# Performance work log

Measured on AMD Instinct MI355X. Metric: run time of the kernel, lower is better.

The kernel has to match this reference:

```python
import jax, jax.numpy as jnp
import numpy as np

D_IN = 1024
D_OUT = 1024
NUM_HEADS = 16
HEAD_DIM = D_OUT // NUM_HEADS


def setup_inputs() -> dict:
    key = jax.random.key(0)
    ks = jax.random.split(key, 6)
    s = 0.02
    return {
        "x": jax.random.normal(ks[0], (4, 2048, D_IN), dtype=jnp.float32),
        "W_q": jax.random.normal(ks[1], (D_IN, D_OUT), dtype=jnp.float32) * s,
        "W_k": jax.random.normal(ks[2], (D_IN, D_OUT), dtype=jnp.float32) * s,
        "W_v": jax.random.normal(ks[3], (D_IN, D_OUT), dtype=jnp.float32) * s,
        "W_o": jax.random.normal(ks[4], (D_OUT, D_OUT), dtype=jnp.float32) * s,
        "b_o": jax.random.normal(ks[5], (D_OUT,), dtype=jnp.float32) * s,
    }


def reference(x, W_q, W_k, W_v, W_o, b_o):
    b, n, _ = x.shape
    # project and split heads: [b, h, n, d]
    q = (x @ W_q).reshape(b, n, NUM_HEADS, HEAD_DIM).transpose(0, 2, 1, 3)
    k = (x @ W_k).reshape(b, n, NUM_HEADS, HEAD_DIM).transpose(0, 2, 1, 3)
    v = (x @ W_v).reshape(b, n, NUM_HEADS, HEAD_DIM).transpose(0, 2, 1, 3)
    scores = jnp.einsum("bhqd,bhkd->bhqk", q, k)
    causal = jnp.tril(jnp.ones((n, n), dtype=bool))  # True = keep
    scores = jnp.where(causal, scores, -jnp.inf)
    attn = jax.nn.softmax(scores / np.sqrt(HEAD_DIM).astype(np.float32), axis=-1)
    ctx = jnp.einsum("bhqk,bhkd->bhqd", attn, v)
    ctx = ctx.transpose(0, 2, 1, 3).reshape(b, n, D_OUT)
    return ctx @ W_o + b_o
```

## Files before the change

kernel.cpp:

```cpp
#include <hip/hip_runtime.h>
#include <hip/hip_bf16.h>

#define NHEADS 16
#define HDIM 64
#define SEQ 2048
#define BATCH 4
#define DMODEL 1024
#define MTOT (BATCH * SEQ)

typedef short v8s __attribute__((ext_vector_type(8)));
typedef short v4s __attribute__((ext_vector_type(4)));
typedef float v4f __attribute__((ext_vector_type(4)));
typedef float v16f __attribute__((ext_vector_type(16)));
typedef unsigned int v4u __attribute__((ext_vector_type(4)));
typedef unsigned short u16;
typedef unsigned int u32;

__device__ __forceinline__ u16 f2bf(float f) {
    union { float f; unsigned u; } v; v.f = f;
    unsigned r = v.u + 0x7FFFu + ((v.u >> 16) & 1u);
    return (u16)(r >> 16);
}

__device__ __forceinline__ void g2l16(const u16* g, short* l) {
    __builtin_amdgcn_global_load_lds(
        (const __attribute__((address_space(1))) u32*)g,
        (__attribute__((address_space(3))) u32*)l, 16, 0, 0);
}

__device__ __forceinline__ unsigned pk_bf16(float a, float b) {
    unsigned r;
    asm("v_cvt_pk_bf16_f32 %0, %1, %2" : "=v"(r) : "v"(a), "v"(b));
    return r;
}
__device__ __forceinline__ void pl32swap(unsigned& x, unsigned& y) {
    asm("v_permlane32_swap_b32 %0, %1" : "+v"(x), "+v"(y));
}
__device__ __forceinline__ v8s build_pa(float a0, float a1, float a2, float a3,
                                        float b0, float b1, float b2, float b3) {
    unsigned X  = pk_bf16(a0, a1);
    unsigned X2 = pk_bf16(a2, a3);
    unsigned Y  = pk_bf16(b0, b1);
    unsigned Y2 = pk_bf16(b2, b3);
    pl32swap(X, Y);
    pl32swap(X2, Y2);
    v4u w; w[0] = X; w[1] = X2; w[2] = Y; w[3] = Y2;
    return __builtin_bit_cast(v8s, w);
}

__device__ __forceinline__ void transpose_body(
    const float* __restrict__ src, u16* __restrict__ dst, int k0, int n0)
{
    __shared__ __align__(8) short Ts[64 * 68];
    const int t = threadIdx.x;
    const int n4 = (t & 15) * 4, kl = t >> 4;
#pragma unroll
    for (int it = 0; it < 4; ++it) {
        int k = kl + 16 * it;
        v4f v = *(const v4f*)&src[(size_t)(k0 + k) * DMODEL + n0 + n4];
        v4s p;
#pragma unroll
        for (int e = 0; e < 4; ++e) p[e] = (short)f2bf(v[e]);
        *(v4s*)&Ts[k * 68 + n4] = p;
    }
    __syncthreads();
    const int nl = t >> 4, k4 = (t & 15) * 4;
#pragma unroll
    for (int it = 0; it < 4; ++it) {
        int n = nl + 16 * it;
        v4s o;
#pragma unroll
        for (int e = 0; e < 4; ++e) o[e] = Ts[(k4 + e) * 68 + n];
        *(v4s*)&dst[(size_t)(n0 + n) * DMODEL + k0 + k4] = o;
    }
}

__global__ __launch_bounds__(256)
void transpose_w(const float* __restrict__ src, u16* __restrict__ dst)
{
    transpose_body(src, dst, blockIdx.x * 64, blockIdx.y * 64);
}

__global__ __launch_bounds__(256)
void prep(const float* __restrict__ x, u16* __restrict__ xb,
          const float* __restrict__ s0, const float* __restrict__ s1,
          const float* __restrict__ s2, const float* __restrict__ s3,
          u16* __restrict__ wdst)
{
    const int blk = blockIdx.x;
    if (blk < 1024) {
        const int z = blk >> 8;
        const int rem = blk & 255;
        const float* src = (z == 0) ? s0 : (z == 1) ? s1 : (z == 2) ? s2 : s3;
        transpose_body(src, wdst + (size_t)z * DMODEL * DMODEL,
                       (rem & 15) * 64, (rem >> 4) * 64);
    } else {
        size_t i = ((size_t)(blk - 1024) * 256 + threadIdx.x) * 8;
        v4f a = *(const v4f*)&x[i];
        v4f b = *(const v4f*)&x[i + 4];
        v8s p;
#pragma unroll
        for (int e = 0; e < 4; ++e) p[e] = (short)f2bf(a[e]);
#pragma unroll
        for (int e = 0; e < 4; ++e) p[4 + e] = (short)f2bf(b[e]);
        *(v8s*)&xb[i] = p;
    }
}

#define QSCALE (0.125f * 1.44269504088896f)

__device__ __forceinline__ void qkv_epilogue(
    v4f (&acc)[4][4], int which, int n0, int m0, int wn, int wm,
    int l15, int quad, u16* Qb, u16* Kb, u16* Vt)
{
    if (which == 2) {
#pragma unroll
        for (int i = 0; i < 4; ++i)
#pragma unroll
            for (int j = 0; j < 4; ++j) {
                int col = n0 + wn + j * 16 + l15;
                int h = col >> 6, d = col & 63;
                int m = m0 + wm + i * 16 + quad * 4;
                int b = m >> 11, n = m & (SEQ - 1);
                v4s pv;
#pragma unroll
                for (int r = 0; r < 4; ++r) pv[r] = (short)f2bf(acc[i][j][r]);
                *(v4s*)&Vt[((size_t)(b * NHEADS + h) * HDIM + d) * SEQ + n] = pv;
            }
    } else {
        u16* Ob = (which == 0) ? Qb : Kb;
        const float scale = (which == 0) ? QSCALE : 1.0f;
#pragma unroll
        for (int i = 0; i < 4; ++i)
#pragma unroll
            for (int j = 0; j < 4; ++j) {
                int col = n0 + wn + j * 16 + l15;
                int h = col >> 6, d = col & 63;
#pragma unroll
                for (int r = 0; r < 4; ++r) {
                    int m = m0 + wm + i * 16 + quad * 4 + r;
                    int b = m >> 11, n = m & (SEQ - 1);
                    Ob[((size_t)(b * NHEADS + h) * SEQ + n) * HDIM + d] =
                        f2bf(acc[i][j][r] * scale);
                }
            }
    }
}

__global__ __launch_bounds__(256, 2)
void qkv_fast(const u16* __restrict__ xb, const u16* __restrict__ Wt,
              u16* __restrict__ Qb, u16* __restrict__ Kb, u16* __restrict__ Vt)
{
    __shared__ __align__(16) short As[128 * 128];
    __shared__ __align__(16) short Bs[128 * 128];

    const int which = blockIdx.z;
    const u16* W = Wt + (size_t)which * DMODEL * DMODEL;

    const int n0 = blockIdx.x * 128;
    const int m0 = blockIdx.y * 128;
    const int t = threadIdx.x;
    const int lane = t & 63;
    const int l15 = lane & 15;
    const int quad = lane >> 4;
    const int wave = t >> 6;
    const int wm = (wave >> 1) * 64;
    const int wn = (wave & 1) * 64;
    const int srow = t >> 4;
    const int sc8 = (t & 15) * 8;

    v4f acc[4][4];
#pragma unroll
    for (int i = 0; i < 4; ++i)
#pragma unroll
        for (int j = 0; j < 4; ++j) acc[i][j] = {0.f, 0.f, 0.f, 0.f};

    for (int k0 = 0; k0 < DMODEL; k0 += 128) {
        __syncthreads();
#pragma unroll
        for (int c = 0; c < 8; ++c) {
            g2l16(&xb[(size_t)(m0 + c * 16 + srow) * DMODEL + k0 + sc8],
                  &As[(c * 16 + srow) * 128 + sc8]);
            g2l16(&W[(size_t)(n0 + c * 16 + srow) * DMODEL + k0 + sc8],
                  &Bs[(c * 16 + srow) * 128 + sc8]);
        }
        __syncthreads();

#pragma unroll
        for (int kh = 0; kh < 4; ++kh) {
            v8s af[4], bf[4];
#pragma unroll
            for (int i = 0; i < 4; ++i)
                af[i] = *(const v8s*)
                    &As[(wm + i * 16 + l15) * 128 + kh * 32 + quad * 8];
#pragma unroll
            for (int j = 0; j < 4; ++j)
                bf[j] = *(const v8s*)
                    &Bs[(wn + j * 16 + l15) * 128 + kh * 32 + quad * 8];
#pragma unroll
            for (int i = 0; i < 4; ++i)
#pragma unroll
                for (int j = 0; j < 4; ++j)
                    acc[i][j] = __builtin_amdgcn_mfma_f32_16x16x32_bf16(
                        af[i], bf[j], acc[i][j], 0, 0, 0);
        }
    }
    qkv_epilogue(acc, which, n0, m0, wn, wm, l15, quad, Qb, Kb, Vt);
}

__global__ __launch_bounds__(256, 2)
void qkv_slow(const float* __restrict__ x, const u16* __restrict__ Wt,
              u16* __restrict__ Qb, u16* __restrict__ Kb, u16* __restrict__ Vt)
{
    __shared__ __align__(16) short As[128 * 32];
    __shared__ __align__(16) short Bs[128 * 32];

    const int which = blockIdx.z;
    const u16* W = Wt + (size_t)which * DMODEL * DMODEL;

    const int n0 = blockIdx.x * 128;
    const int m0 = blockIdx.y * 128;
    const int t = threadIdx.x;
    const int lane = t & 63;
    const int l15 = lane & 15;
    const int quad = lane >> 4;
    const int wave = t >> 6;
    const int wm = (wave >> 1) * 64;
    const int wn = (wave & 1) * 64;
    const int srow = t >> 2;
    const int sc8 = (t & 3) * 8;

    v4f acc[4][4];
#pragma unroll
    for (int i = 0; i < 4; ++i)
#pragma unroll
        for (int j = 0; j < 4; ++j) acc[i][j] = {0.f, 0.f, 0.f, 0.f};

    for (int k0 = 0; k0 < DMODEL; k0 += 32) {
        __syncthreads();
        g2l16(&W[(size_t)(n0 + srow) * DMODEL + k0 + sc8], &Bs[srow * 32 + sc8]);
        g2l16(&W[(size_t)(n0 + 64 + srow) * DMODEL + k0 + sc8],
              &Bs[(64 + srow) * 32 + sc8]);
#pragma unroll
        for (int it = 0; it < 2; ++it) {
            int row = srow + 64 * it;
            const float* xp = &x[(size_t)(m0 + row) * DMODEL + k0 + sc8];
            v4f x0 = *(const v4f*)xp;
            v4f x1 = *(const v4f*)(xp + 4);
            v8s av;
#pragma unroll
            for (int e = 0; e < 4; ++e) av[e] = (short)f2bf(x0[e]);
#pragma unroll
            for (int e = 0; e < 4; ++e) av[4 + e] = (short)f2bf(x1[e]);
            *(v8s*)&As[row * 32 + sc8] = av;
        }
        __syncthreads();

        v8s af[4], bf[4];
#pragma unroll
        for (int i = 0; i < 4; ++i)
            af[i] = *(const v8s*)&As[(wm + i * 16 + l15) * 32 + quad * 8];
#pragma unroll
        for (int j = 0; j < 4; ++j)
            bf[j] = *(const v8s*)&Bs[(wn + j * 16 + l15) * 32 + quad * 8];
#pragma unroll
        for (int i = 0; i < 4; ++i)
#pragma unroll
            for (int j = 0; j < 4; ++j)
                acc[i][j] = __builtin_amdgcn_mfma_f32_16x16x32_bf16(
                    af[i], bf[j], acc[i][j], 0, 0, 0);
    }
    qkv_epilogue(acc, which, n0, m0, wn, wm, l15, quad, Qb, Kb, Vt);
}

#define VXOR(d) ((((d) & 7) << 1) | (((d) >> 3) & 1))

__global__ __launch_bounds__(256, 2)
void attn(const u16* __restrict__ Qb, const u16* __restrict__ Kb,
          const u16* __restrict__ Vt, u16* __restrict__ Cx)
{
    __shared__ __align__(16) short Ks[128 * 64];
    __shared__ __align__(16) short Vs[64 * 128];

    const int ell = blockIdx.x;
    const int xcd = ell & 7;
    const int rest = ell >> 3;
    const int p = rest & 7;
    const int bh = ((rest >> 3) << 3) | xcd;

    const int t = threadIdx.x;
    const int lane = t & 63;
    const int l31 = lane & 31;
    const int hi = lane >> 5;
    const int wave = t >> 6;
    const int koff = hi * 8;

    const u16* Qh = Qb + (size_t)bh * SEQ * HDIM;
    const u16* Kh = Kb + (size_t)bh * SEQ * HDIM;
    const u16* Vh = Vt + (size_t)bh * HDIM * SEQ;

    const int krow = t >> 3;
    const int kslot = t & 7;
    const int vrow = t >> 4;
    const int vslot = t & 15;
    const int b = bh >> 4, h = bh & 15;

#pragma unroll 1
    for (int phase = 0; phase < 2; ++phase) {
        const int qt = phase ? p : (15 - p);
        const int q0w = qt * 128 + wave * 32;

        v8s qf[4];
#pragma unroll
        for (int dc = 0; dc < 4; ++dc)
            qf[dc] = *(const v8s*)
                &Qh[(size_t)(q0w + l31) * HDIM + dc * 16 + koff];

        v16f o0, o1;
#pragma unroll
        for (int r = 0; r < 16; ++r) { o0[r] = 0.f; o1[r] = 0.f; }
        float ls = 0.f;

        v8s pk[4], pv[4];
#pragma unroll
        for (int it = 0; it < 4; ++it)
            pk[it] = *(const v8s*)
                &Kh[(size_t)(it * 32 + krow) * HDIM + kslot * 8];
#pragma unroll
        for (int it = 0; it < 4; ++it)
            pv[it] = *(const v8s*)
                &Vh[(size_t)(it * 16 + vrow) * SEQ + vslot * 8];

#pragma unroll 1
        for (int kb = 0; kb <= qt; ++kb) {
            __syncthreads();
#pragma unroll
            for (int it = 0; it < 4; ++it) {
                int row = it * 32 + krow;
                *(v8s*)&Ks[row * 64 + ((kslot ^ (row & 7)) << 3)] = pk[it];
            }
#pragma unroll
            for (int it = 0; it < 4; ++it) {
                int d = it * 16 + vrow;
                *(v8s*)&Vs[d * 128 + ((vslot ^ VXOR(d)) << 3)] = pv[it];
            }
            __syncthreads();

            if (kb < qt) {
                const int kn = (kb + 1) * 128;
#pragma unroll
                for (int it = 0; it < 4; ++it)
                    pk[it] = *(const v8s*)
                        &Kh[(size_t)(kn + it * 32 + krow) * HDIM + kslot * 8];
#pragma unroll
                for (int it = 0; it < 4; ++it)
                    pv[it] = *(const v8s*)
                        &Vh[(size_t)(it * 16 + vrow) * SEQ + kn + vslot * 8];
            }

#pragma unroll
            for (int k2 = 0; k2 < 2; ++k2) {
                const int kbase = kb * 128 + k2 * 64;
                if (kbase > q0w + 31) continue;
                const bool diag = (kbase + 63 > q0w);
                const int qrow = q0w + l31;

                v16f st0, st1;
#pragma unroll
                for (int r = 0; r < 16; ++r) { st0[r] = 0.f; st1[r] = 0.f; }
#pragma unroll
                for (int dc = 0; dc < 4; ++dc) {
                    const int ds = dc * 2 + hi;
                    const int r0 = k2 * 64 + l31;
                    const int r1 = k2 * 64 + 32 + l31;
                    v8s kf0 = *(const v8s*)
                        &Ks[r0 * 64 + ((ds ^ (r0 & 7)) << 3)];
                    v8s kf1 = *(const v8s*)
                        &Ks[r1 * 64 + ((ds ^ (r1 & 7)) << 3)];
                    st0 = __builtin_amdgcn_mfma_f32_32x32x16_bf16(
                        kf0, qf[dc], st0, 0, 0, 0);
                    st1 = __builtin_amdgcn_mfma_f32_32x32x16_bf16(
                        kf1, qf[dc], st1, 0, 0, 0);
                }

                v16f pe0, pe1;
                if (!diag) {
#pragma unroll
                    for (int r = 0; r < 16; ++r) {
                        pe0[r] = exp2f(st0[r]);
                        pe1[r] = exp2f(st1[r]);
                    }
                } else {
#pragma unroll
                    for (int r = 0; r < 16; ++r) {
                        int kl = kbase + (r & 3) + 8 * (r >> 2) + 4 * hi;
                        pe0[r] = (kl > qrow) ? 0.f : exp2f(st0[r]);
                        pe1[r] = (kl + 32 > qrow) ? 0.f : exp2f(st1[r]);
                    }
                }
#pragma unroll
                for (int r = 0; r < 16; ++r) ls += pe0[r] + pe1[r];

                v8s pa0 = build_pa(pe0[0], pe0[1], pe0[2], pe0[3],
                                   pe0[4], pe0[5], pe0[6], pe0[7]);
                v8s pa1 = build_pa(pe0[8], pe0[9], pe0[10], pe0[11],
                                   pe0[12], pe0[13], pe0[14], pe0[15]);
                v8s pa2 = build_pa(pe1[0], pe1[1], pe1[2], pe1[3],
                                   pe1[4], pe1[5], pe1[6], pe1[7]);
                v8s pa3 = build_pa(pe1[8], pe1[9], pe1[10], pe1[11],
                                   pe1[12], pe1[13], pe1[14], pe1[15]);

#pragma unroll
                for (int kc = 0; kc < 4; ++kc) {
                    v8s pav = (kc == 0) ? pa0 : (kc == 1) ? pa1
                              : (kc == 2) ? pa2 : pa3;
                    const int ks = k2 * 8 + kc * 2 + hi;
                    const int d0 = l31, d1 = 32 + l31;
                    v8s vf0 = *(const v8s*)
                        &Vs[d0 * 128 + ((ks ^ VXOR(d0)) << 3)];
                    v8s vf1 = *(const v8s*)
                        &Vs[d1 * 128 + ((ks ^ VXOR(d1)) << 3)];
                    o0 = __builtin_amdgcn_mfma_f32_32x32x16_bf16(
                        pav, vf0, o0, 0, 0, 0);
                    o1 = __builtin_amdgcn_mfma_f32_32x32x16_bf16(
                        pav, vf1, o1, 0, 0, 0);
                }
            }
        }

        ls += __shfl_xor(ls, 32, 64);
        float inv = 1.f / ls;
#pragma unroll
        for (int r = 0; r < 16; ++r) {
            int m = (r & 3) + 8 * (r >> 2) + 4 * hi;
            float im = __shfl(inv, m, 64);
            size_t idx = ((size_t)(b * SEQ + q0w + m)) * DMODEL
                         + h * HDIM + l31;
            Cx[idx] = f2bf(o0[r] * im);
            Cx[idx + 32] = f2bf(o1[r] * im);
        }
    }
}

__global__ __launch_bounds__(256, 2)
void out_gemm(const u16* __restrict__ Cx, const u16* __restrict__ WoT,
              const float* __restrict__ bo, float* __restrict__ Y)
{
    __shared__ __align__(16) short As[128 * 64];
    __shared__ __align__(16) short Bs[128 * 64];

    const int n0 = blockIdx.x * 128;
    const int m0 = blockIdx.y * 128;
    const int t = threadIdx.x;
    const int lane = t & 63;
    const int l15 = lane & 15;
    const int quad = lane >> 4;
    const int wave = t >> 6;
    const int wm = (wave >> 1) * 64;
    const int wn = (wave & 1) * 64;
    const int srow = t >> 3;
    const int sc8 = (t & 7) * 8;

    v4f acc[4][4];
#pragma unroll
    for (int i = 0; i < 4; ++i)
#pragma unroll
        for (int j = 0; j < 4; ++j) acc[i][j] = {0.f, 0.f, 0.f, 0.f};

    for (int k0 = 0; k0 < DMODEL; k0 += 64) {
        __syncthreads();
#pragma unroll
        for (int c = 0; c < 4; ++c) {
            g2l16(&Cx[(size_t)(m0 + c * 32 + srow) * DMODEL + k0 + sc8],
                  &As[(c * 32 + srow) * 64 + sc8]);
            g2l16(&WoT[(size_t)(n0 + c * 32 + srow) * DMODEL + k0 + sc8],
                  &Bs[(c * 32 + srow) * 64 + sc8]);
        }
        __syncthreads();

#pragma unroll
        for (int kh = 0; kh < 2; ++kh) {
            v8s af[4], bf[4];
#pragma unroll
            for (int i = 0; i < 4; ++i)
                af[i] = *(const v8s*)
                    &As[(wm + i * 16 + l15) * 64 + kh * 32 + quad * 8];
#pragma unroll
            for (int j = 0; j < 4; ++j)
                bf[j] = *(const v8s*)
                    &Bs[(wn + j * 16 + l15) * 64 + kh * 32 + quad * 8];
#pragma unroll
            for (int i = 0; i < 4; ++i)
#pragma unroll
                for (int j = 0; j < 4; ++j)
                    acc[i][j] = __builtin_amdgcn_mfma_f32_16x16x32_bf16(
                        af[i], bf[j], acc[i][j], 0, 0, 0);
        }
    }

#pragma unroll
    for (int i = 0; i < 4; ++i)
#pragma unroll
        for (int j = 0; j < 4; ++j) {
            int col = n0 + wn + j * 16 + l15;
            float bias = bo[col];
#pragma unroll
            for (int r = 0; r < 4; ++r) {
                int m = m0 + wm + i * 16 + quad * 4 + r;
                Y[(size_t)m * DMODEL + col] = acc[i][j][r] + bias;
            }
        }
}

extern "C" void kernel_launch(void* const* d_in, const int* in_sizes, int n_in,
                              void* d_out, int out_size, void* d_ws,
                              size_t ws_size, hipStream_t stream)
{
    const float* x  = (const float*)d_in[0];
    const float* Wq = (const float*)d_in[1];
    const float* Wk = (const float*)d_in[2];
    const float* Wv = (const float*)d_in[3];
    const float* Wo = (const float*)d_in[4];
    const float* bo = (const float*)d_in[5];
    float* Y = (float*)d_out;

    const size_t per = (size_t)BATCH * NHEADS * SEQ * HDIM;
    const size_t wsz = (size_t)DMODEL * DMODEL;
    u16* base = (u16*)d_ws;

    if (ws_size >= (size_t)72 * 1024 * 1024) {
        u16* xb  = base;
        u16* Cx  = base;
        u16* Wt4 = base + per;
        u16* Qb  = base + per + 4 * wsz;
        u16* Kb  = Qb + per;
        u16* Vt  = Kb + per;

        prep<<<1024 + MTOT * DMODEL / (256 * 8), 256, 0, stream>>>(
            x, xb, Wq, Wk, Wv, Wo, Wt4);
        qkv_fast<<<dim3(DMODEL / 128, MTOT / 128, 3), 256, 0, stream>>>(
            xb, Wt4, Qb, Kb, Vt);
        attn<<<512, 256, 0, stream>>>(Qb, Kb, Vt, Cx);
        out_gemm<<<dim3(DMODEL / 128, MTOT / 128), 256, 0, stream>>>(
            Cx, Wt4 + 3 * wsz, bo, Y);
    } else {
        u16* Wt  = base;
        u16* Cx  = base;
        u16* Qb  = base + per;
        u16* WoT = base + per;
        u16* Kb  = base + 2 * per;
        u16* Vt  = base + 3 * per;

        transpose_w<<<dim3(16, 16), 256, 0, stream>>>(Wq, Wt);
        transpose_w<<<dim3(16, 16), 256, 0, stream>>>(Wk, Wt + wsz);
        transpose_w<<<dim3(16, 16), 256, 0, stream>>>(Wv, Wt + 2 * wsz);
        qkv_slow<<<dim3(DMODEL / 128, MTOT / 128, 3), 256, 0, stream>>>(
            x, Wt, Qb, Kb, Vt);
        attn<<<512, 256, 0, stream>>>(Qb, Kb, Vt, Cx);
        transpose_w<<<dim3(16, 16), 256, 0, stream>>>(Wo, WoT);
        out_gemm<<<dim3(DMODEL / 128, MTOT / 128), 256, 0, stream>>>(
            Cx, WoT, bo, Y);
    }
}
```

Before: 295.0 us.

## Triple-buffer QKV GEMM with async loads, swizzled LDS, 256x128 tiles

Rewrites the QKV projection GEMM to use 512-thread blocks computing 256x128 tiles. Operands are streamed through a three-stage LDS ring buffer in 64-wide K chunks, with vmcnt waits so global-to-LDS copies for upcoming stages overlap the MFMA work. LDS columns are XOR-swizzled to avoid bank conflicts, and wave priority is raised around the MFMA block. This removes the serialized load-then-compute barriers of the old loop, at the cost of higher LDS use (one block per CU) and hand-tuned waitcnt logic that depends on how g2l16 issues its loads.

```diff
diff --git a/kernel.cpp b/kernel.cpp
--- a/kernel.cpp
+++ b/kernel.cpp
@@ -147,18 +147,41 @@
     }
 }
 
-__global__ __launch_bounds__(256, 2)
+#define QKV_ABUF (256 * 64)
+#define QKV_BBUF (128 * 64)
+
+__device__ __forceinline__ void qkv_stage(
+    const u16* __restrict__ xb, const u16* __restrict__ W,
+    int m0, int t, int s, short* As3, short* Bs3)
+{
+    const int srr = t >> 3;
+    const int scol = ((t & 7) ^ (srr & 7)) * 8;
+    short* A = As3 + (s % 3) * QKV_ABUF;
+    short* B = Bs3 + (s % 3) * QKV_BBUF;
+    const int k0 = s * 64;
+#pragma unroll
+    for (int c = 0; c < 4; ++c)
+        g2l16(&xb[(size_t)(m0 + c * 64 + srr) * DMODEL + k0 + scol],
+              &A[(c * 64 + srr) * 64 + (t & 7) * 8]);
+#pragma unroll
+    for (int c = 0; c < 2; ++c)
+        g2l16(&W[(size_t)(c * 64 + srr) * DMODEL + k0 + scol],
+              &B[(c * 64 + srr) * 64 + (t & 7) * 8]);
+}
+
+__global__ __launch_bounds__(512, 1)
 void qkv_fast(const u16* __restrict__ xb, const u16* __restrict__ Wt,
               u16* __restrict__ Qb, u16* __restrict__ Kb, u16* __restrict__ Vt)
 {
-    __shared__ __align__(16) short As[128 * 128];
-    __shared__ __align__(16) short Bs[128 * 128];
-
-    const int which = blockIdx.z;
-    const u16* W = Wt + (size_t)which * DMODEL * DMODEL;
-
-    const int n0 = blockIdx.x * 128;
-    const int m0 = blockIdx.y * 128;
+    __shared__ __align__(16) short As3[3 * QKV_ABUF];
+    __shared__ __align__(16) short Bs3[3 * QKV_BBUF];
+
+    const int bx = blockIdx.x;
+    const int which = bx >> 3;
+    const int n0 = (bx & 7) * 128;
+    const int m0 = blockIdx.y * 256;
+    const u16* W = Wt + (size_t)which * DMODEL * DMODEL + (size_t)n0 * DMODEL;
+
     const int t = threadIdx.x;
     const int lane = t & 63;
     const int l15 = lane & 15;
@@ -166,8 +189,6 @@
     const int wave = t >> 6;
     const int wm = (wave >> 1) * 64;
     const int wn = (wave & 1) * 64;
-    const int srow = t >> 4;
-    const int sc8 = (t & 15) * 8;
 
     v4f acc[4][4];
 #pragma unroll
@@ -175,36 +196,45 @@
 #pragma unroll
         for (int j = 0; j < 4; ++j) acc[i][j] = {0.f, 0.f, 0.f, 0.f};
 
-    for (int k0 = 0; k0 < DMODEL; k0 += 128) {
+    qkv_stage(xb, W, m0, t, 0, As3, Bs3);
+    qkv_stage(xb, W, m0, t, 1, As3, Bs3);
+
+#pragma unroll 1
+    for (int tt = 0; tt < 16; ++tt) {
+        if (tt < 15) asm volatile("s_waitcnt vmcnt(6)" ::: "memory");
+        else         asm volatile("s_waitcnt vmcnt(0)" ::: "memory");
+        __builtin_amdgcn_sched_barrier(0);
         __syncthreads();
-#pragma unroll
-        for (int c = 0; c < 8; ++c) {
-            g2l16(&xb[(size_t)(m0 + c * 16 + srow) * DMODEL + k0 + sc8],
-                  &As[(c * 16 + srow) * 128 + sc8]);
-            g2l16(&W[(size_t)(n0 + c * 16 + srow) * DMODEL + k0 + sc8],
-                  &Bs[(c * 16 + srow) * 128 + sc8]);
-        }
-        __syncthreads();
-
-#pragma unroll
-        for (int kh = 0; kh < 4; ++kh) {
-            v8s af[4], bf[4];
-#pragma unroll
-            for (int i = 0; i < 4; ++i)
-                af[i] = *(const v8s*)
-                    &As[(wm + i * 16 + l15) * 128 + kh * 32 + quad * 8];
+
+        if (tt + 2 < 16) qkv_stage(xb, W, m0, t, tt + 2, As3, Bs3);
+
+        const short* A = As3 + (tt % 3) * QKV_ABUF;
+        const short* B = Bs3 + (tt % 3) * QKV_BBUF;
+        v8s af[4][2], bf[4][2];
+#pragma unroll
+        for (int i = 0; i < 4; ++i)
+#pragma unroll
+            for (int kh = 0; kh < 2; ++kh)
+                af[i][kh] = *(const v8s*)&A[(wm + i * 16 + l15) * 64 +
+                                            (((kh * 4 + quad) ^ (l15 & 7)) << 3)];
+#pragma unroll
+        for (int j = 0; j < 4; ++j)
+#pragma unroll
+            for (int kh = 0; kh < 2; ++kh)
+                bf[j][kh] = *(const v8s*)&B[(wn + j * 16 + l15) * 64 +
+                                            (((kh * 4 + quad) ^ (l15 & 7)) << 3)];
+        __builtin_amdgcn_s_setprio(1);
+#pragma unroll
+        for (int i = 0; i < 4; ++i)
 #pragma unroll
             for (int j = 0; j < 4; ++j)
-                bf[j] = *(const v8s*)
-                    &Bs[(wn + j * 16 + l15) * 128 + kh * 32 + quad * 8];
-#pragma unroll
-            for (int i = 0; i < 4; ++i)
-#pragma unroll
-                for (int j = 0; j < 4; ++j)
+#pragma unroll
+                for (int kh = 0; kh < 2; ++kh)
                     acc[i][j] = __builtin_amdgcn_mfma_f32_16x16x32_bf16(
-                        af[i], bf[j], acc[i][j], 0, 0, 0);
-        }
-    }
+                        af[i][kh], bf[j][kh], acc[i][j], 0, 0, 0);
+        __builtin_amdgcn_s_setprio(0);
+    }
+
     qkv_epilogue(acc, which, n0, m0, wn, wm, l15, quad, Qb, Kb, Vt);
 }
 
@@ -538,7 +568,7 @@
 
         prep<<<1024 + MTOT * DMODEL / (256 * 8), 256, 0, stream>>>(
             x, xb, Wq, Wk, Wv, Wo, Wt4);
-        qkv_fast<<<dim3(DMODEL / 128, MTOT / 128, 3), 256, 0, stream>>>(
+        qkv_fast<<<dim3(24, MTOT / 256), 512, 0, stream>>>(
             xb, Wt4, Qb, Kb, Vt);
         attn<<<512, 256, 0, stream>>>(Qb, Kb, Vt, Cx);
         out_gemm<<<dim3(DMODEL / 128, MTOT / 128), 256, 0, stream>>>(
```

After: 261.2 us. -11.4%, faster.
